# Kernel tuning notes

Hardware: AMD Instinct MI355X
Metric: run time of the kernel (lower is better)

Reference implementation:

```python
import jax, jax.numpy as jnp
import numpy as np

N = 8192      # total factor-graph rows (detection nodes + association nodes)
ND = N // 2   # detection-node rows; rest are association (edge) rows
D_RAW = 74    # raw input dim; last 10 cols = convex hull (5 points x 2 coords)
EPS = 1e-5    # BatchNorm eps


def _adjs():
    # signed factor-graph adjacencies with self-loops marking row type
    rng = np.random.RandomState(0)
    deg = 8
    node_adj = np.zeros((N, N), np.float32)
    edge_adj = np.zeros((N, N), np.float32)
    nbr = rng.randint(ND, N, size=(ND, deg))
    node_adj[np.repeat(np.arange(ND), deg), nbr.ravel()] = rng.choice([-1.0, 1.0], ND * deg).astype(np.float32)
    node_adj[np.arange(ND), np.arange(ND)] = 1.0
    nbr2 = rng.randint(0, ND, size=(N - ND, deg))
    edge_adj[np.repeat(np.arange(ND, N), deg), nbr2.ravel()] = rng.choice([-1.0, 1.0], (N - ND) * deg).astype(np.float32)
    edge_adj[np.arange(ND, N), np.arange(ND, N)] = 1.0
    return jnp.asarray(node_adj), jnp.asarray(edge_adj)


def setup_inputs() -> dict:
    key = jax.random.key(0)
    ks = jax.random.split(key, 16)
    node_adj, edge_adj = _adjs()

    def lin(k, fi, fo):
        return jax.random.normal(k, (fi, fo), jnp.float32) / np.sqrt(fi)

    inp = {"x": jax.random.normal(ks[0], (N, D_RAW), jnp.float32),
           "node_adj": node_adj, "edge_adj": edge_adj}
    # PointNetfeatsmall: 1x1 conv stack 3->16->32->64 with eval-mode BatchNorm
    for i, (fi, fo) in enumerate([(3, 16), (16, 32), (32, 64)], 1):
        k = jax.random.split(ks[i], 5)
        inp[f"pn_w{i}"] = lin(k[0], fi, fo)
        inp[f"pn_b{i}"] = 0.1 * jax.random.normal(k[1], (fo,), jnp.float32)
        inp[f"pn_g{i}"] = 1.0 + 0.1 * jax.random.normal(k[2], (fo,), jnp.float32)
        inp[f"pn_be{i}"] = 0.1 * jax.random.normal(k[3], (fo,), jnp.float32)
        inp[f"pn_m{i}"] = 0.1 * jax.random.normal(k[4], (fo,), jnp.float32)
        inp[f"pn_v{i}"] = jnp.ones((fo,), jnp.float32)
    # FactorGraphConvolution weights (msg_type='concat' -> in dim doubles)
    for i, (fi, fo) in enumerate([(256, 64), (128, 64), (128, 1)], 1):
        k = jax.random.split(ks[10 + i], 2)
        inp[f"gc{i}_wn"] = lin(k[0], fi, fo)
        inp[f"gc{i}_we"] = lin(k[1], fi, fo)
        inp[f"gc{i}_bn"] = jnp.zeros((fo,), jnp.float32)
        inp[f"gc{i}_be"] = jnp.zeros((fo,), jnp.float32)
    inp["gc3_bn"] = jnp.full((1,), -4.595, jnp.float32)  # nn.init.constant_ in TrackMPNN.__init__
    inp["gc3_be"] = jnp.full((1,), 4.595, jnp.float32)
    return inp


def _bn(h, g, b, m, v):  # h: [N, C, P], eval-mode BatchNorm1d
    return (h - m[:, None]) * (g[:, None] / jnp.sqrt(v[:, None] + EPS)) + b[:, None]


def _fgc(h, node_adj, edge_adj, wn, we, bn_, be_, relu):
    # concat(self, aggregated-neighbors) -> linear; node/edge rows use their own branch
    node_out = jnp.concatenate([h, node_adj @ h], axis=1) @ wn + bn_
    edge_out = jnp.concatenate([h, edge_adj @ h], axis=1) @ we + be_
    out = jnp.where((jnp.diag(node_adj) != 0)[:, None], node_out, edge_out)
    return jax.nn.relu(out) if relu else out


def reference(x, node_adj, edge_adj,
              pn_w1, pn_b1, pn_g1, pn_be1, pn_m1, pn_v1,
              pn_w2, pn_b2, pn_g2, pn_be2, pn_m2, pn_v2,
              pn_w3, pn_b3, pn_g3, pn_be3, pn_m3, pn_v3,
              gc1_wn, gc1_we, gc1_bn, gc1_be,
              gc2_wn, gc2_we, gc2_bn, gc2_be,
              gc3_wn, gc3_we, gc3_bn, gc3_be):
    # convex hull branch: [N, 3, 5] (third coordinate zero-padded)
    ch = jnp.concatenate([x[:, -10:].reshape(-1, 2, 5),
                          jnp.zeros((x.shape[0], 1, 5), x.dtype)], axis=1)
    h = jax.nn.relu(_bn(jnp.einsum('ncp,cd->ndp', ch, pn_w1) + pn_b1[:, None], pn_g1, pn_be1, pn_m1, pn_v1))
    h = jax.nn.relu(_bn(jnp.einsum('ncp,cd->ndp', h, pn_w2) + pn_b2[:, None], pn_g2, pn_be2, pn_m2, pn_v2))
    h = _bn(jnp.einsum('ncp,cd->ndp', h, pn_w3) + pn_b3[:, None], pn_g3, pn_be3, pn_m3, pn_v3)
    feat = h.max(axis=2)                       # PointNet global max pool -> [N, 64]
    h = jnp.concatenate([x[:, :-10], feat], axis=1)  # [N, 128]
    h = _fgc(h, node_adj, edge_adj, gc1_wn, gc1_we, gc1_bn, gc1_be, True)
    h = _fgc(h, node_adj, edge_adj, gc2_wn, gc2_we, gc2_bn, gc2_be, True)
    h = _fgc(h, node_adj, edge_adj, gc3_wn, gc3_we, gc3_bn, gc3_be, False)
    return jax.nn.sigmoid(h)                   # [N, 1]
```

## Files before the change

kernel.cpp:

```cpp
#include <hip/hip_runtime.h>
#include <math.h>

#define NROWS 8192
#define NDET  4096


static constexpr int OFF_SGN = 65536;
static constexpr int OFF_FW  = 131072;
static constexpr int OFF_H3  = 135168;
static constexpr int OFF_H0  = 2756608;
static constexpr int OFF_AGG = 3805184;
static constexpr int OFF_H1  = 4853760;
static constexpr int OFF_H2  = 5378048;

__global__ void k_fold(const float* __restrict__ w1, const float* __restrict__ b1,
                       const float* __restrict__ g1, const float* __restrict__ be1,
                       const float* __restrict__ m1, const float* __restrict__ v1,
                       const float* __restrict__ w2, const float* __restrict__ b2,
                       const float* __restrict__ g2, const float* __restrict__ be2,
                       const float* __restrict__ m2, const float* __restrict__ v2,
                       const float* __restrict__ w3, const float* __restrict__ b3,
                       const float* __restrict__ g3, const float* __restrict__ be3,
                       const float* __restrict__ m3, const float* __restrict__ v3,
                       float* __restrict__ fw)
{
    int t = threadIdx.x;
    for (int i = t; i < 48; i += 256) { int d = i & 15; fw[i]       = w1[i] * g1[d] * rsqrtf(v1[d] + 1e-5f); }
    for (int i = t; i < 16; i += 256) {                 fw[48 + i]  = (b1[i] - m1[i]) * g1[i] * rsqrtf(v1[i] + 1e-5f) + be1[i]; }
    for (int i = t; i < 512; i += 256){ int d = i & 31; fw[64 + i]  = w2[i] * g2[d] * rsqrtf(v2[d] + 1e-5f); }
    for (int i = t; i < 32; i += 256) {                 fw[576 + i] = (b2[i] - m2[i]) * g2[i] * rsqrtf(v2[i] + 1e-5f) + be2[i]; }
    for (int i = t; i < 2048; i += 256){int d = i & 63; fw[608 + i] = w3[i] * g3[d] * rsqrtf(v3[d] + 1e-5f); }
    for (int i = t; i < 64; i += 256) {                 fw[2656 + i]= (b3[i] - m3[i]) * g3[i] * rsqrtf(v3[i] + 1e-5f) + be3[i]; }
}

__global__ void k_extract(const float* __restrict__ nodeA, const float* __restrict__ edgeA,
                          int* __restrict__ idxT, float* __restrict__ sgnT)
{
    int row = blockIdx.x, t = threadIdx.x;
    const float* src; int col0, fill;
    if (row < NDET) { src = nodeA + (size_t)row * NROWS + NDET; col0 = NDET; fill = NDET; }
    else            { src = edgeA + (size_t)row * NROWS;        col0 = 0;    fill = 0;    }
    __shared__ int scnt;
    if (t == 0) scnt = 0;
    __syncthreads();
    const float4* s4 = (const float4*)src;
    #pragma unroll
    for (int it = 0; it < 4; ++it) {
        float4 v = s4[t + it * 256];
        int cb = col0 + (t + it * 256) * 4;
        if (v.x != 0.f) { int p = atomicAdd(&scnt, 1); idxT[p * NROWS + row] = cb;     sgnT[p * NROWS + row] = v.x; }
        if (v.y != 0.f) { int p = atomicAdd(&scnt, 1); idxT[p * NROWS + row] = cb + 1; sgnT[p * NROWS + row] = v.y; }
        if (v.z != 0.f) { int p = atomicAdd(&scnt, 1); idxT[p * NROWS + row] = cb + 2; sgnT[p * NROWS + row] = v.z; }
        if (v.w != 0.f) { int p = atomicAdd(&scnt, 1); idxT[p * NROWS + row] = cb + 3; sgnT[p * NROWS + row] = v.w; }
    }
    __syncthreads();
    for (int p = scnt + t; p < 8; p += 256) { idxT[p * NROWS + row] = fill; sgnT[p * NROWS + row] = 0.f; }
}

__global__ void k_pointnet(const float* __restrict__ x, const float* __restrict__ fw,
                           float* __restrict__ h3buf)
{
    int lane = threadIdx.x & 63;
    int p    = threadIdx.x >> 6;
    int row  = blockIdx.x * 64 + lane;
    float a0 = x[row * 74 + 64 + p];
    float a1 = x[row * 74 + 69 + p];
    const float* fw1 = fw;        const float* fb1 = fw + 48;
    const float* fw2 = fw + 64;   const float* fb2 = fw + 576;
    const float* fw3 = fw + 608;  const float* fb3 = fw + 2656;
    float h1[16];
    #pragma unroll
    for (int d = 0; d < 16; ++d)
        h1[d] = fmaxf(0.f, a0 * fw1[d] + a1 * fw1[16 + d] + fb1[d]);
    float h2[32];
    #pragma unroll
    for (int e = 0; e < 32; ++e) {
        float s = fb2[e];
        #pragma unroll
        for (int d = 0; d < 16; ++d) s += h1[d] * fw2[d * 32 + e];
        h2[e] = fmaxf(0.f, s);
    }
    for (int f = 0; f < 64; ++f) {
        float s = fb3[f];
        #pragma unroll
        for (int e = 0; e < 32; ++e) s += h2[e] * fw3[e * 64 + f];
        h3buf[(p * 64 + f) * NROWS + row] = s;
    }
}

__global__ void k_assemble(const float* __restrict__ x, const float* __restrict__ h3buf,
                           float* __restrict__ h0T)
{
    int g = blockIdx.x * 256 + threadIdx.x;
    int k = g >> 13, row = g & 8191;
    float v;
    if (k < 64) v = x[row * 74 + k];
    else {
        int f = k - 64;
        v = h3buf[f * NROWS + row];
        #pragma unroll
        for (int p = 1; p < 5; ++p) v = fmaxf(v, h3buf[(p * 64 + f) * NROWS + row]);
    }
    h0T[k * NROWS + row] = v;
}

template<int F>
__global__ void k_gather(const float* __restrict__ hT, const int* __restrict__ idxT,
                         const float* __restrict__ sgnT, float* __restrict__ aggT)
{
    int g = blockIdx.x * 256 + threadIdx.x;
    int k = g >> 13, row = g & 8191;
    const float* hk = hT + (size_t)k * NROWS;
    float acc = hk[row];
    #pragma unroll
    for (int j = 0; j < 8; ++j) {
        int nb   = idxT[j * NROWS + row];
        float sg = sgnT[j * NROWS + row];
        acc += sg * hk[nb];
    }
    aggT[k * NROWS + row] = acc;
}

template<int F, bool RELU>
__global__ void k_gemm(const float* __restrict__ hT, const float* __restrict__ aggT,
                       const float* __restrict__ wn, const float* __restrict__ we,
                       const float* __restrict__ bn, const float* __restrict__ be,
                       float* __restrict__ outT)
{
    int row = blockIdx.x * 256 + threadIdx.x;
    int d0  = blockIdx.y * 4;
    bool isnode = (blockIdx.x < 16);
    const float* W = isnode ? wn : we;
    const float* B = isnode ? bn : be;
    float acc[4];
    #pragma unroll
    for (int dd = 0; dd < 4; ++dd) acc[dd] = B[d0 + dd];
    #pragma unroll
    for (int half = 0; half < 2; ++half) {
        const float* src = half ? aggT : hT;
        const float* Wh  = W + half * F * 64;
        for (int k0 = 0; k0 < F; k0 += 8) {
            float in[8];
            #pragma unroll
            for (int kk = 0; kk < 8; ++kk) in[kk] = src[(size_t)(k0 + kk) * NROWS + row];
            #pragma unroll
            for (int kk = 0; kk < 8; ++kk)
                #pragma unroll
                for (int dd = 0; dd < 4; ++dd)
                    acc[dd] += in[kk] * Wh[(k0 + kk) * 64 + d0 + dd];
        }
    }
    #pragma unroll
    for (int dd = 0; dd < 4; ++dd) {
        float v = acc[dd];
        if (RELU) v = fmaxf(v, 0.f);
        outT[(size_t)(d0 + dd) * NROWS + row] = v;
    }
}

__global__ void k_gc3(const float* __restrict__ h2T, const float* __restrict__ aggT,
                      const float* __restrict__ wn, const float* __restrict__ we,
                      const float* __restrict__ bn, const float* __restrict__ be,
                      float* __restrict__ out)
{
    int row = blockIdx.x * 256 + threadIdx.x;
    bool isnode = row < NDET;
    const float* w = isnode ? wn : we;
    float acc = isnode ? bn[0] : be[0];
    #pragma unroll 8
    for (int k = 0; k < 64; ++k) acc += h2T[(size_t)k * NROWS + row] * w[k];
    #pragma unroll 8
    for (int k = 0; k < 64; ++k) acc += aggT[(size_t)k * NROWS + row] * w[64 + k];
    out[row] = 1.f / (1.f + expf(-acc));
}

extern "C" void kernel_launch(void* const* d_in, const int* in_sizes, int n_in,
                              void* d_out, int out_size, void* d_ws, size_t ws_size,
                              hipStream_t stream)
{
    const float* x      = (const float*)d_in[0];
    const float* nodeA  = (const float*)d_in[1];
    const float* edgeA  = (const float*)d_in[2];
    const float* pw1 = (const float*)d_in[3];  const float* pb1 = (const float*)d_in[4];
    const float* pg1 = (const float*)d_in[5];  const float* pe1 = (const float*)d_in[6];
    const float* pm1 = (const float*)d_in[7];  const float* pv1 = (const float*)d_in[8];
    const float* pw2 = (const float*)d_in[9];  const float* pb2 = (const float*)d_in[10];
    const float* pg2 = (const float*)d_in[11]; const float* pe2 = (const float*)d_in[12];
    const float* pm2 = (const float*)d_in[13]; const float* pv2 = (const float*)d_in[14];
    const float* pw3 = (const float*)d_in[15]; const float* pb3 = (const float*)d_in[16];
    const float* pg3 = (const float*)d_in[17]; const float* pe3 = (const float*)d_in[18];
    const float* pm3 = (const float*)d_in[19]; const float* pv3 = (const float*)d_in[20];
    const float* g1wn = (const float*)d_in[21]; const float* g1we = (const float*)d_in[22];
    const float* g1bn = (const float*)d_in[23]; const float* g1be = (const float*)d_in[24];
    const float* g2wn = (const float*)d_in[25]; const float* g2we = (const float*)d_in[26];
    const float* g2bn = (const float*)d_in[27]; const float* g2be = (const float*)d_in[28];
    const float* g3wn = (const float*)d_in[29]; const float* g3we = (const float*)d_in[30];
    const float* g3bn = (const float*)d_in[31]; const float* g3be = (const float*)d_in[32];

    float* ws   = (float*)d_ws;
    int*   idxT = (int*)ws;
    float* sgnT = ws + OFF_SGN;
    float* fw   = ws + OFF_FW;
    float* h3   = ws + OFF_H3;
    float* h0T  = ws + OFF_H0;
    float* aggT = ws + OFF_AGG;
    float* h1T  = ws + OFF_H1;
    float* h2T  = ws + OFF_H2;
    float* out  = (float*)d_out;

    k_fold<<<1, 256, 0, stream>>>(pw1, pb1, pg1, pe1, pm1, pv1,
                                  pw2, pb2, pg2, pe2, pm2, pv2,
                                  pw3, pb3, pg3, pe3, pm3, pv3, fw);
    k_extract<<<NROWS, 256, 0, stream>>>(nodeA, edgeA, idxT, sgnT);
    k_pointnet<<<128, 320, 0, stream>>>(x, fw, h3);
    k_assemble<<<4096, 256, 0, stream>>>(x, h3, h0T);

    k_gather<128><<<4096, 256, 0, stream>>>(h0T, idxT, sgnT, aggT);
    k_gemm<128, true><<<dim3(32, 16), 256, 0, stream>>>(h0T, aggT, g1wn, g1we, g1bn, g1be, h1T);

    k_gather<64><<<2048, 256, 0, stream>>>(h1T, idxT, sgnT, aggT);
    k_gemm<64, true><<<dim3(32, 16), 256, 0, stream>>>(h1T, aggT, g2wn, g2we, g2bn, g2be, h2T);

    k_gather<64><<<2048, 256, 0, stream>>>(h2T, idxT, sgnT, aggT);
    k_gc3<<<32, 256, 0, stream>>>(h2T, aggT, g3wn, g3we, g3bn, g3be, out);
}
```

Before: 583.6 us.

## Switch activations to row-major and fuse pointnet max-pool, fold, and final aggregation

Activations and neighbour lists move from column-major to row-major, so each gather pulls whole contiguous 64-float neighbour rows per wavefront. The BatchNorm fold moves into the pointnet kernel's shared memory, and the max over points is taken in registers. This removes the fold and assemble kernels and the h3 buffer. The first layer reads x and the pointnet features directly instead of a packed h0. The last layer fuses its aggregation with a wave-reduced dot product. The costs are more redundant pointnet work per block (layers 1-2 are recomputed for each feature group) and strided x reads in the GEMM.

```diff
diff --git a/kernel.cpp b/kernel.cpp
--- a/kernel.cpp
+++ b/kernel.cpp
@@ -4,42 +4,19 @@
 #define NROWS 8192
 #define NDET  4096
 
-
 static constexpr int OFF_SGN = 65536;
-static constexpr int OFF_FW  = 131072;
-static constexpr int OFF_H3  = 135168;
-static constexpr int OFF_H0  = 2756608;
-static constexpr int OFF_AGG = 3805184;
-static constexpr int OFF_H1  = 4853760;
-static constexpr int OFF_H2  = 5378048;
-
-__global__ void k_fold(const float* __restrict__ w1, const float* __restrict__ b1,
-                       const float* __restrict__ g1, const float* __restrict__ be1,
-                       const float* __restrict__ m1, const float* __restrict__ v1,
-                       const float* __restrict__ w2, const float* __restrict__ b2,
-                       const float* __restrict__ g2, const float* __restrict__ be2,
-                       const float* __restrict__ m2, const float* __restrict__ v2,
-                       const float* __restrict__ w3, const float* __restrict__ b3,
-                       const float* __restrict__ g3, const float* __restrict__ be3,
-                       const float* __restrict__ m3, const float* __restrict__ v3,
-                       float* __restrict__ fw)
-{
-    int t = threadIdx.x;
-    for (int i = t; i < 48; i += 256) { int d = i & 15; fw[i]       = w1[i] * g1[d] * rsqrtf(v1[d] + 1e-5f); }
-    for (int i = t; i < 16; i += 256) {                 fw[48 + i]  = (b1[i] - m1[i]) * g1[i] * rsqrtf(v1[i] + 1e-5f) + be1[i]; }
-    for (int i = t; i < 512; i += 256){ int d = i & 31; fw[64 + i]  = w2[i] * g2[d] * rsqrtf(v2[d] + 1e-5f); }
-    for (int i = t; i < 32; i += 256) {                 fw[576 + i] = (b2[i] - m2[i]) * g2[i] * rsqrtf(v2[i] + 1e-5f) + be2[i]; }
-    for (int i = t; i < 2048; i += 256){int d = i & 63; fw[608 + i] = w3[i] * g3[d] * rsqrtf(v3[d] + 1e-5f); }
-    for (int i = t; i < 64; i += 256) {                 fw[2656 + i]= (b3[i] - m3[i]) * g3[i] * rsqrtf(v3[i] + 1e-5f) + be3[i]; }
-}
+static constexpr int OFF_PN  = 131072;
+static constexpr int OFF_AGG = 655360;
+static constexpr int OFF_H1  = 1703936;
+static constexpr int OFF_H2  = 2228224;
 
 __global__ void k_extract(const float* __restrict__ nodeA, const float* __restrict__ edgeA,
-                          int* __restrict__ idxT, float* __restrict__ sgnT)
+                          int* __restrict__ idx, float* __restrict__ sgn)
 {
     int row = blockIdx.x, t = threadIdx.x;
-    const float* src; int col0, fill;
-    if (row < NDET) { src = nodeA + (size_t)row * NROWS + NDET; col0 = NDET; fill = NDET; }
-    else            { src = edgeA + (size_t)row * NROWS;        col0 = 0;    fill = 0;    }
+    const float* src; int col0;
+    if (row < NDET) { src = nodeA + (size_t)row * NROWS + NDET; col0 = NDET; }
+    else            { src = edgeA + (size_t)row * NROWS;        col0 = 0;    }
     __shared__ int scnt;
     if (t == 0) scnt = 0;
     __syncthreads();
@@ -48,139 +25,235 @@
     for (int it = 0; it < 4; ++it) {
         float4 v = s4[t + it * 256];
         int cb = col0 + (t + it * 256) * 4;
-        if (v.x != 0.f) { int p = atomicAdd(&scnt, 1); idxT[p * NROWS + row] = cb;     sgnT[p * NROWS + row] = v.x; }
-        if (v.y != 0.f) { int p = atomicAdd(&scnt, 1); idxT[p * NROWS + row] = cb + 1; sgnT[p * NROWS + row] = v.y; }
-        if (v.z != 0.f) { int p = atomicAdd(&scnt, 1); idxT[p * NROWS + row] = cb + 2; sgnT[p * NROWS + row] = v.z; }
-        if (v.w != 0.f) { int p = atomicAdd(&scnt, 1); idxT[p * NROWS + row] = cb + 3; sgnT[p * NROWS + row] = v.w; }
+        if (v.x != 0.f) { int p = atomicAdd(&scnt, 1); idx[row * 8 + p] = cb;     sgn[row * 8 + p] = v.x; }
+        if (v.y != 0.f) { int p = atomicAdd(&scnt, 1); idx[row * 8 + p] = cb + 1; sgn[row * 8 + p] = v.y; }
+        if (v.z != 0.f) { int p = atomicAdd(&scnt, 1); idx[row * 8 + p] = cb + 2; sgn[row * 8 + p] = v.z; }
+        if (v.w != 0.f) { int p = atomicAdd(&scnt, 1); idx[row * 8 + p] = cb + 3; sgn[row * 8 + p] = v.w; }
     }
     __syncthreads();
-    for (int p = scnt + t; p < 8; p += 256) { idxT[p * NROWS + row] = fill; sgnT[p * NROWS + row] = 0.f; }
-}
-
-__global__ void k_pointnet(const float* __restrict__ x, const float* __restrict__ fw,
-                           float* __restrict__ h3buf)
+    for (int p = scnt + t; p < 8; p += 256) { idx[row * 8 + p] = 0; sgn[row * 8 + p] = 0.f; }
+}
+
+__global__ void k_pointnet(const float* __restrict__ x,
+                           const float* __restrict__ w1, const float* __restrict__ b1,
+                           const float* __restrict__ g1, const float* __restrict__ be1,
+                           const float* __restrict__ m1, const float* __restrict__ v1,
+                           const float* __restrict__ w2, const float* __restrict__ b2,
+                           const float* __restrict__ g2, const float* __restrict__ be2,
+                           const float* __restrict__ m2, const float* __restrict__ v2,
+                           const float* __restrict__ w3, const float* __restrict__ b3,
+                           const float* __restrict__ g3, const float* __restrict__ be3,
+                           const float* __restrict__ m3, const float* __restrict__ v3,
+                           float* __restrict__ pn)
+{
+    __shared__ float fw[2720];
+    int t = threadIdx.x;
+    for (int i = t; i < 48; i += 256)  { int d = i & 15; fw[i]       = w1[i] * g1[d] * rsqrtf(v1[d] + 1e-5f); }
+    for (int i = t; i < 16; i += 256)  {                 fw[48 + i]  = (b1[i] - m1[i]) * g1[i] * rsqrtf(v1[i] + 1e-5f) + be1[i]; }
+    for (int i = t; i < 512; i += 256) { int d = i & 31; fw[64 + i]  = w2[i] * g2[d] * rsqrtf(v2[d] + 1e-5f); }
+    for (int i = t; i < 32; i += 256)  {                 fw[576 + i] = (b2[i] - m2[i]) * g2[i] * rsqrtf(v2[i] + 1e-5f) + be2[i]; }
+    for (int i = t; i < 2048; i += 256){ int d = i & 63; fw[608 + i] = w3[i] * g3[d] * rsqrtf(v3[d] + 1e-5f); }
+    for (int i = t; i < 64; i += 256)  {                 fw[2656 + i]= (b3[i] - m3[i]) * g3[i] * rsqrtf(v3[i] + 1e-5f) + be3[i]; }
+    __syncthreads();
+
+    int lane = t & 63, fsub = t >> 6;
+    int row  = blockIdx.x * 64 + lane;
+    int f0   = (blockIdx.y * 4 + fsub) * 4;
+
+    float vmax[4] = {-3.0e38f, -3.0e38f, -3.0e38f, -3.0e38f};
+    for (int p = 0; p < 5; ++p) {
+        float a0 = x[(size_t)row * 74 + 64 + p];
+        float a1 = x[(size_t)row * 74 + 69 + p];
+        float h1[16];
+        #pragma unroll
+        for (int d = 0; d < 16; ++d)
+            h1[d] = fmaxf(0.f, a0 * fw[d] + a1 * fw[16 + d] + fw[48 + d]);
+        float h2[32];
+        #pragma unroll
+        for (int e = 0; e < 32; ++e) {
+            float s = fw[576 + e];
+            #pragma unroll
+            for (int d = 0; d < 16; ++d) s += h1[d] * fw[64 + d * 32 + e];
+            h2[e] = fmaxf(0.f, s);
+        }
+        #pragma unroll
+        for (int ff = 0; ff < 4; ++ff) {
+            float s = fw[2656 + f0 + ff];
+            #pragma unroll
+            for (int e = 0; e < 32; ++e) s += h2[e] * fw[608 + e * 64 + f0 + ff];
+            vmax[ff] = fmaxf(vmax[ff], s);
+        }
+    }
+    float4 o; o.x = vmax[0]; o.y = vmax[1]; o.z = vmax[2]; o.w = vmax[3];
+    *(float4*)&pn[(size_t)row * 64 + f0] = o;
+}
+
+__global__ void k_gather1(const float* __restrict__ x, const float* __restrict__ pn,
+                          const int* __restrict__ idx, const float* __restrict__ sgn,
+                          float* __restrict__ agg)
 {
     int lane = threadIdx.x & 63;
-    int p    = threadIdx.x >> 6;
-    int row  = blockIdx.x * 64 + lane;
-    float a0 = x[row * 74 + 64 + p];
-    float a1 = x[row * 74 + 69 + p];
-    const float* fw1 = fw;        const float* fb1 = fw + 48;
-    const float* fw2 = fw + 64;   const float* fb2 = fw + 576;
-    const float* fw3 = fw + 608;  const float* fb3 = fw + 2656;
-    float h1[16];
-    #pragma unroll
-    for (int d = 0; d < 16; ++d)
-        h1[d] = fmaxf(0.f, a0 * fw1[d] + a1 * fw1[16 + d] + fb1[d]);
-    float h2[32];
-    #pragma unroll
-    for (int e = 0; e < 32; ++e) {
-        float s = fb2[e];
-        #pragma unroll
-        for (int d = 0; d < 16; ++d) s += h1[d] * fw2[d * 32 + e];
-        h2[e] = fmaxf(0.f, s);
-    }
-    for (int f = 0; f < 64; ++f) {
-        float s = fb3[f];
-        #pragma unroll
-        for (int e = 0; e < 32; ++e) s += h2[e] * fw3[e * 64 + f];
-        h3buf[(p * 64 + f) * NROWS + row] = s;
-    }
-}
-
-__global__ void k_assemble(const float* __restrict__ x, const float* __restrict__ h3buf,
-                           float* __restrict__ h0T)
-{
-    int g = blockIdx.x * 256 + threadIdx.x;
-    int k = g >> 13, row = g & 8191;
-    float v;
-    if (k < 64) v = x[row * 74 + k];
-    else {
-        int f = k - 64;
-        v = h3buf[f * NROWS + row];
-        #pragma unroll
-        for (int p = 1; p < 5; ++p) v = fmaxf(v, h3buf[(p * 64 + f) * NROWS + row]);
-    }
-    h0T[k * NROWS + row] = v;
-}
-
-template<int F>
-__global__ void k_gather(const float* __restrict__ hT, const int* __restrict__ idxT,
-                         const float* __restrict__ sgnT, float* __restrict__ aggT)
-{
-    int g = blockIdx.x * 256 + threadIdx.x;
-    int k = g >> 13, row = g & 8191;
-    const float* hk = hT + (size_t)k * NROWS;
-    float acc = hk[row];
+    int row  = blockIdx.x * 4 + (threadIdx.x >> 6);
+    float acc0 = x[(size_t)row * 74 + lane];
+    float acc1 = pn[(size_t)row * 64 + lane];
     #pragma unroll
     for (int j = 0; j < 8; ++j) {
-        int nb   = idxT[j * NROWS + row];
-        float sg = sgnT[j * NROWS + row];
-        acc += sg * hk[nb];
-    }
-    aggT[k * NROWS + row] = acc;
-}
-
-template<int F, bool RELU>
-__global__ void k_gemm(const float* __restrict__ hT, const float* __restrict__ aggT,
-                       const float* __restrict__ wn, const float* __restrict__ we,
-                       const float* __restrict__ bn, const float* __restrict__ be,
-                       float* __restrict__ outT)
-{
-    int row = blockIdx.x * 256 + threadIdx.x;
-    int d0  = blockIdx.y * 4;
-    bool isnode = (blockIdx.x < 16);
+        int nb   = idx[row * 8 + j];
+        float sg = sgn[row * 8 + j];
+        acc0 += sg * x[(size_t)nb * 74 + lane];
+        acc1 += sg * pn[(size_t)nb * 64 + lane];
+    }
+    agg[(size_t)row * 128 + lane]      = acc0;
+    agg[(size_t)row * 128 + 64 + lane] = acc1;
+}
+
+__global__ void k_gather2(const float* __restrict__ h, const int* __restrict__ idx,
+                          const float* __restrict__ sgn, float* __restrict__ agg)
+{
+    int lane = threadIdx.x & 63;
+    int row  = blockIdx.x * 4 + (threadIdx.x >> 6);
+    float acc = h[(size_t)row * 64 + lane];
+    #pragma unroll
+    for (int j = 0; j < 8; ++j) {
+        int nb   = idx[row * 8 + j];
+        float sg = sgn[row * 8 + j];
+        acc += sg * h[(size_t)nb * 64 + lane];
+    }
+    agg[(size_t)row * 64 + lane] = acc;
+}
+
+__global__ void k_gemm1(const float* __restrict__ x, const float* __restrict__ pn,
+                        const float* __restrict__ agg,
+                        const float* __restrict__ wn, const float* __restrict__ we,
+                        const float* __restrict__ bn, const float* __restrict__ be,
+                        float* __restrict__ out)
+{
+    int r_l = threadIdx.x >> 2, cg = threadIdx.x & 3;
+    int row = blockIdx.x * 64 + r_l;
+    int c0  = blockIdx.y * 16 + cg * 4;
+    bool isnode = blockIdx.x < 64;
     const float* W = isnode ? wn : we;
     const float* B = isnode ? bn : be;
-    float acc[4];
-    #pragma unroll
-    for (int dd = 0; dd < 4; ++dd) acc[dd] = B[d0 + dd];
-    #pragma unroll
-    for (int half = 0; half < 2; ++half) {
-        const float* src = half ? aggT : hT;
-        const float* Wh  = W + half * F * 64;
-        for (int k0 = 0; k0 < F; k0 += 8) {
-            float in[8];
-            #pragma unroll
-            for (int kk = 0; kk < 8; ++kk) in[kk] = src[(size_t)(k0 + kk) * NROWS + row];
-            #pragma unroll
-            for (int kk = 0; kk < 8; ++kk)
-                #pragma unroll
-                for (int dd = 0; dd < 4; ++dd)
-                    acc[dd] += in[kk] * Wh[(k0 + kk) * 64 + d0 + dd];
-        }
-    }
-    #pragma unroll
-    for (int dd = 0; dd < 4; ++dd) {
-        float v = acc[dd];
-        if (RELU) v = fmaxf(v, 0.f);
-        outT[(size_t)(d0 + dd) * NROWS + row] = v;
-    }
-}
-
-__global__ void k_gc3(const float* __restrict__ h2T, const float* __restrict__ aggT,
+    float acc[4] = {B[c0], B[c0 + 1], B[c0 + 2], B[c0 + 3]};
+
+    const float2* x2 = (const float2*)(x + (size_t)row * 74);
+    #pragma unroll
+    for (int kg = 0; kg < 32; ++kg) {
+        float2 v = x2[kg];
+        float4 wv0 = *(const float4*)&W[(kg * 2) * 64 + c0];
+        float4 wv1 = *(const float4*)&W[(kg * 2 + 1) * 64 + c0];
+        acc[0] += v.x * wv0.x + v.y * wv1.x;
+        acc[1] += v.x * wv0.y + v.y * wv1.y;
+        acc[2] += v.x * wv0.z + v.y * wv1.z;
+        acc[3] += v.x * wv0.w + v.y * wv1.w;
+    }
+    const float4* p4 = (const float4*)(pn + (size_t)row * 64);
+    #pragma unroll
+    for (int kg = 0; kg < 16; ++kg) {
+        float4 v = p4[kg];
+        const float* vv = &v.x;
+        #pragma unroll
+        for (int kk = 0; kk < 4; ++kk) {
+            float4 wv = *(const float4*)&W[(64 + kg * 4 + kk) * 64 + c0];
+            acc[0] += vv[kk] * wv.x; acc[1] += vv[kk] * wv.y;
+            acc[2] += vv[kk] * wv.z; acc[3] += vv[kk] * wv.w;
+        }
+    }
+    const float4* a4 = (const float4*)(agg + (size_t)row * 128);
+    #pragma unroll
+    for (int kg = 0; kg < 32; ++kg) {
+        float4 v = a4[kg];
+        const float* vv = &v.x;
+        #pragma unroll
+        for (int kk = 0; kk < 4; ++kk) {
+            float4 wv = *(const float4*)&W[(128 + kg * 4 + kk) * 64 + c0];
+            acc[0] += vv[kk] * wv.x; acc[1] += vv[kk] * wv.y;
+            acc[2] += vv[kk] * wv.z; acc[3] += vv[kk] * wv.w;
+        }
+    }
+    float4 o;
+    o.x = fmaxf(acc[0], 0.f); o.y = fmaxf(acc[1], 0.f);
+    o.z = fmaxf(acc[2], 0.f); o.w = fmaxf(acc[3], 0.f);
+    *(float4*)&out[(size_t)row * 64 + c0] = o;
+}
+
+__global__ void k_gemm2(const float* __restrict__ h, const float* __restrict__ agg,
+                        const float* __restrict__ wn, const float* __restrict__ we,
+                        const float* __restrict__ bn, const float* __restrict__ be,
+                        float* __restrict__ out)
+{
+    int r_l = threadIdx.x >> 2, cg = threadIdx.x & 3;
+    int row = blockIdx.x * 64 + r_l;
+    int c0  = blockIdx.y * 16 + cg * 4;
+    bool isnode = blockIdx.x < 64;
+    const float* W = isnode ? wn : we;
+    const float* B = isnode ? bn : be;
+    float acc[4] = {B[c0], B[c0 + 1], B[c0 + 2], B[c0 + 3]};
+
+    const float4* h4 = (const float4*)(h + (size_t)row * 64);
+    const float4* a4 = (const float4*)(agg + (size_t)row * 64);
+    #pragma unroll
+    for (int kg = 0; kg < 16; ++kg) {
+        float4 v = h4[kg];
+        const float* vv = &v.x;
+        #pragma unroll
+        for (int kk = 0; kk < 4; ++kk) {
+            float4 wv = *(const float4*)&W[(kg * 4 + kk) * 64 + c0];
+            acc[0] += vv[kk] * wv.x; acc[1] += vv[kk] * wv.y;
+            acc[2] += vv[kk] * wv.z; acc[3] += vv[kk] * wv.w;
+        }
+    }
+    #pragma unroll
+    for (int kg = 0; kg < 16; ++kg) {
+        float4 v = a4[kg];
+        const float* vv = &v.x;
+        #pragma unroll
+        for (int kk = 0; kk < 4; ++kk) {
+            float4 wv = *(const float4*)&W[(64 + kg * 4 + kk) * 64 + c0];
+            acc[0] += vv[kk] * wv.x; acc[1] += vv[kk] * wv.y;
+            acc[2] += vv[kk] * wv.z; acc[3] += vv[kk] * wv.w;
+        }
+    }
+    float4 o;
+    o.x = fmaxf(acc[0], 0.f); o.y = fmaxf(acc[1], 0.f);
+    o.z = fmaxf(acc[2], 0.f); o.w = fmaxf(acc[3], 0.f);
+    *(float4*)&out[(size_t)row * 64 + c0] = o;
+}
+
+__global__ void k_gc3(const float* __restrict__ h2, const int* __restrict__ idx,
+                      const float* __restrict__ sgn,
                       const float* __restrict__ wn, const float* __restrict__ we,
                       const float* __restrict__ bn, const float* __restrict__ be,
                       float* __restrict__ out)
 {
-    int row = blockIdx.x * 256 + threadIdx.x;
+    int lane = threadIdx.x & 63;
+    int row  = blockIdx.x * 4 + (threadIdx.x >> 6);
+    float own = h2[(size_t)row * 64 + lane];
+    float agg = own;
+    #pragma unroll
+    for (int j = 0; j < 8; ++j) {
+        int nb   = idx[row * 8 + j];
+        float sg = sgn[row * 8 + j];
+        agg += sg * h2[(size_t)nb * 64 + lane];
+    }
     bool isnode = row < NDET;
     const float* w = isnode ? wn : we;
-    float acc = isnode ? bn[0] : be[0];
-    #pragma unroll 8
-    for (int k = 0; k < 64; ++k) acc += h2T[(size_t)k * NROWS + row] * w[k];
-    #pragma unroll 8
-    for (int k = 0; k < 64; ++k) acc += aggT[(size_t)k * NROWS + row] * w[64 + k];
-    out[row] = 1.f / (1.f + expf(-acc));
+    float bias = isnode ? bn[0] : be[0];
+    float acc = own * w[lane] + agg * w[64 + lane];
+    #pragma unroll
+    for (int off = 32; off > 0; off >>= 1)
+        acc += __shfl_xor(acc, off, 64);
+    if (lane == 0)
+        out[row] = 1.f / (1.f + expf(-(acc + bias)));
 }
 
 extern "C" void kernel_launch(void* const* d_in, const int* in_sizes, int n_in,
                               void* d_out, int out_size, void* d_ws, size_t ws_size,
                               hipStream_t stream)
 {
-    const float* x      = (const float*)d_in[0];
-    const float* nodeA  = (const float*)d_in[1];
-    const float* edgeA  = (const float*)d_in[2];
+    const float* x     = (const float*)d_in[0];
+    const float* nodeA = (const float*)d_in[1];
+    const float* edgeA = (const float*)d_in[2];
     const float* pw1 = (const float*)d_in[3];  const float* pb1 = (const float*)d_in[4];
     const float* pg1 = (const float*)d_in[5];  const float* pe1 = (const float*)d_in[6];
     const float* pm1 = (const float*)d_in[7];  const float* pv1 = (const float*)d_in[8];
@@ -197,30 +270,23 @@
     const float* g3wn = (const float*)d_in[29]; const float* g3we = (const float*)d_in[30];
     const float* g3bn = (const float*)d_in[31]; const float* g3be = (const float*)d_in[32];
 
-    float* ws   = (float*)d_ws;
-    int*   idxT = (int*)ws;
-    float* sgnT = ws + OFF_SGN;
-    float* fw   = ws + OFF_FW;
-    float* h3   = ws + OFF_H3;
-    float* h0T  = ws + OFF_H0;
-    float* aggT = ws + OFF_AGG;
-    float* h1T  = ws + OFF_H1;
-    float* h2T  = ws + OFF_H2;
-    float* out  = (float*)d_out;
-
-    k_fold<<<1, 256, 0, stream>>>(pw1, pb1, pg1, pe1, pm1, pv1,
-                                  pw2, pb2, pg2, pe2, pm2, pv2,
-                                  pw3, pb3, pg3, pe3, pm3, pv3, fw);
-    k_extract<<<NROWS, 256, 0, stream>>>(nodeA, edgeA, idxT, sgnT);
-    k_pointnet<<<128, 320, 0, stream>>>(x, fw, h3);
-    k_assemble<<<4096, 256, 0, stream>>>(x, h3, h0T);
-
-    k_gather<128><<<4096, 256, 0, stream>>>(h0T, idxT, sgnT, aggT);
-    k_gemm<128, true><<<dim3(32, 16), 256, 0, stream>>>(h0T, aggT, g1wn, g1we, g1bn, g1be, h1T);
-
-    k_gather<64><<<2048, 256, 0, stream>>>(h1T, idxT, sgnT, aggT);
-    k_gemm<64, true><<<dim3(32, 16), 256, 0, stream>>>(h1T, aggT, g2wn, g2we, g2bn, g2be, h2T);
-
-    k_gather<64><<<2048, 256, 0, stream>>>(h2T, idxT, sgnT, aggT);
-    k_gc3<<<32, 256, 0, stream>>>(h2T, aggT, g3wn, g3we, g3bn, g3be, out);
-}
+    float* ws  = (float*)d_ws;
+    int*   idx = (int*)ws;
+    float* sgn = ws + OFF_SGN;
+    float* pn  = ws + OFF_PN;
+    float* agg = ws + OFF_AGG;
+    float* h1  = ws + OFF_H1;
+    float* h2  = ws + OFF_H2;
+    float* out = (float*)d_out;
+
+    k_extract<<<NROWS, 256, 0, stream>>>(nodeA, edgeA, idx, sgn);
+    k_pointnet<<<dim3(128, 4), 256, 0, stream>>>(x,
+        pw1, pb1, pg1, pe1, pm1, pv1,
+        pw2, pb2, pg2, pe2, pm2, pv2,
+        pw3, pb3, pg3, pe3, pm3, pv3, pn);
+    k_gather1<<<2048, 256, 0, stream>>>(x, pn, idx, sgn, agg);
+    k_gemm1<<<dim3(128, 4), 256, 0, stream>>>(x, pn, agg, g1wn, g1we, g1bn, g1be, h1);
+    k_gather2<<<2048, 256, 0, stream>>>(h1, idx, sgn, agg);
+    k_gemm2<<<dim3(128, 4), 256, 0, stream>>>(h1, agg, g2wn, g2we, g2bn, g2be, h2);
+    k_gc3<<<2048, 256, 0, stream>>>(h2, idx, sgn, g3wn, g3we, g3bn, g3be, out);
+}
```

After: 1.066 ms. 1.83x slower.
